# Performance work log

Hardware: AMD Instinct MI355X
Metric: run time of the kernel (lower is better)

The kernel has to match this reference:

```python
import jax, jax.numpy as jnp
import numpy as np

N = 100000
DIM = 128
M = 1600000
E = 200000
HOP = 2


def setup_inputs() -> dict:
    key = jax.random.key(0)
    k1, k2, k3, k4 = jax.random.split(key, 4)
    edge = jax.random.randint(k1, (2, E), 0, N, dtype=jnp.int64)
    adj_row = jax.random.randint(k2, (M,), 0, N, dtype=jnp.int64)
    adj_col = jax.random.randint(k3, (M,), 0, N, dtype=jnp.int64)
    # degree consistent with adjacency rows (clamped to >=1 to avoid 1/0)
    deg = jax.ops.segment_sum(jnp.ones((M,), jnp.float32), adj_row, num_segments=N)
    deg = jnp.maximum(deg, 1.0).reshape(N, 1)
    # 'gaussian' signature sampling: row-L2-normalized standard normal vectors
    g = jax.random.normal(k4, (N, DIM), dtype=jnp.float32)
    x_sig = g / jnp.linalg.norm(g, axis=1, keepdims=True)
    return {"edge": edge, "adj_row": adj_row, "adj_col": adj_col, "deg": deg, "x_sig": x_sig}


def reference(edge, adj_row, adj_col, deg, x_sig):
    n = deg.shape[0]
    D = x_sig.shape[1]
    degrev = 1.0 / deg  # [N,1]
    # x: [N, 3*D] -- raw / rsqrt(deg)-scaled / rsqrt(1+log(deg))-scaled signatures
    x = jnp.concatenate(
        [x_sig, x_sig * jax.lax.rsqrt(deg), x_sig * jax.lax.rsqrt(1.0 + jnp.log(deg))],
        axis=1,
    )

    def spmm(v):  # adj_t @ v via gather + segment-sum over nnz
        return jax.ops.segment_sum(v[adj_col], adj_row, num_segments=n)

    xs = [x, degrev * spmm(x)]
    for _ in range(2, HOP + 1):
        xs.append(degrev * spmm(xs[-1]) - xs[-2])
    # [N, K, D] with K = 3*(hop+1)
    X = jnp.concatenate(xs, axis=1).reshape(n, -1, D)
    a = X[edge[0]]  # [E, K, D]
    b = X[edge[1]]  # [E, K, D]
    ret = jnp.einsum("ekd,eld->ekl", a, b)  # [E, K, K]
    ret = ret + jnp.swapaxes(ret, 1, 2)
    return ret.reshape(ret.shape[0], -1)  # [E, K*K]
```

## Files before the change

kernel.cpp:

```cpp
#include <hip/hip_runtime.h>
#include <hip/hip_fp16.h>

#define D128 128
#define X19_STRIDE 768

typedef __attribute__((ext_vector_type(8))) _Float16 f16x8;
typedef __attribute__((ext_vector_type(4))) float    f32x4;

__global__ void k_scales(const float* __restrict__ deg, float* __restrict__ scales, int N) {
  int n = blockIdx.x * blockDim.x + threadIdx.x;
  if (n >= N) return;
  float dg = deg[n];
  scales[2 * n]     = rsqrtf(dg);
  scales[2 * n + 1] = rsqrtf(1.0f + logf(dg));
}

__global__ void k_hist(const int* __restrict__ row, int* __restrict__ cnt, int M) {
  int i = blockIdx.x * blockDim.x + threadIdx.x;
  if (i < M) atomicAdd(&cnt[row[i]], 1);
}

__global__ void __launch_bounds__(256)
k_blocksum(const int* __restrict__ cnt, int* __restrict__ bsum, int n) {
  __shared__ int ws[4];
  int base = blockIdx.x * 1024;
  int t = threadIdx.x;
  int s = 0;
  for (int j = t; j < 1024; j += 256) {
    int i = base + j;
    if (i < n) s += cnt[i];
  }
  #pragma unroll
  for (int d = 32; d >= 1; d >>= 1) s += __shfl_down(s, d);
  if ((t & 63) == 0) ws[t >> 6] = s;
  __syncthreads();
  if (t == 0) bsum[blockIdx.x] = ws[0] + ws[1] + ws[2] + ws[3];
}

__global__ void k_scan_bsums(const int* __restrict__ bsum, int* __restrict__ bpre,
                             int* __restrict__ off, int nb, int n) {
  if (threadIdx.x == 0 && blockIdx.x == 0) {
    int run = 0;
    for (int b = 0; b < nb; ++b) { bpre[b] = run; run += bsum[b]; }
    off[n] = run;
  }
}

__global__ void __launch_bounds__(1024)
k_scan_apply(const int* __restrict__ cnt, const int* __restrict__ bpre,
             int* __restrict__ off, int* __restrict__ cursor, int n) {
  __shared__ int warp_sums[16];
  int i = blockIdx.x * 1024 + threadIdx.x;
  int lane = threadIdx.x & 63;
  int wid  = threadIdx.x >> 6;
  int v = (i < n) ? cnt[i] : 0;
  int s = v;
  #pragma unroll
  for (int d = 1; d < 64; d <<= 1) {
    int t = __shfl_up(s, d);
    if (lane >= d) s += t;
  }
  if (lane == 63) warp_sums[wid] = s;
  __syncthreads();
  if (threadIdx.x < 16) {
    int ws = warp_sums[threadIdx.x];
    #pragma unroll
    for (int d = 1; d < 16; d <<= 1) {
      int t = __shfl_up(ws, d);
      if ((int)threadIdx.x >= d) ws += t;
    }
    warp_sums[threadIdx.x] = ws;
  }
  __syncthreads();
  int excl = (s - v) + (wid > 0 ? warp_sums[wid - 1] : 0) + bpre[blockIdx.x];
  if (i < n) { off[i] = excl; cursor[i] = excl; }
}

__global__ void k_scatter(const int* __restrict__ row, const int* __restrict__ col,
                          int* __restrict__ cursor, int* __restrict__ csr_col, int M) {
  int i = blockIdx.x * blockDim.x + threadIdx.x;
  if (i < M) {
    int r = row[i];
    int pos = atomicAdd(&cursor[r], 1);
    csr_col[pos] = col[i];
  }
}

__global__ void __launch_bounds__(256)
k_spmm1(const float* __restrict__ x_sig, const float* __restrict__ scales,
        __half* __restrict__ X19,
        const int* __restrict__ off, const int* __restrict__ csr_col,
        const float* __restrict__ deg, int N) {
  int r = blockIdx.x * 4 + (threadIdx.x >> 6);
  if (r >= N) return;
  int lane = threadIdx.x & 63;
  int d0 = lane * 2;
  int start = off[r], end = off[r + 1];
  float a0x = 0.f, a0y = 0.f, a1x = 0.f, a1y = 0.f, a2x = 0.f, a2y = 0.f;
  for (int b = start; b < end; b += 64) {
    int len = min(end - b, 64);
    int ci = (lane < len) ? csr_col[b + lane] : 0;
    for (int j = 0; j < len; ++j) {
      int c = __shfl(ci, j);
      float2 v = *reinterpret_cast<const float2*>(x_sig + (size_t)c * D128 + d0);
      float2 s = *reinterpret_cast<const float2*>(scales + 2 * c);
      a0x += v.x;        a0y += v.y;
      a1x += v.x * s.x;  a1y += v.y * s.x;
      a2x += v.x * s.y;  a2y += v.y * s.y;
    }
  }
  float dr = 1.0f / deg[r];
  __half* o = X19 + (size_t)r * X19_STRIDE + d0;
  *reinterpret_cast<__half2*>(o)       = __floats2half2_rn(a0x * dr, a0y * dr);
  *reinterpret_cast<__half2*>(o + 128) = __floats2half2_rn(a1x * dr, a1y * dr);
  *reinterpret_cast<__half2*>(o + 256) = __floats2half2_rn(a2x * dr, a2y * dr);
}

__global__ void __launch_bounds__(256)
k_spmm2(const float* __restrict__ x_sig, const float* __restrict__ scales,
        __half* __restrict__ X19,
        const int* __restrict__ off, const int* __restrict__ csr_col,
        const float* __restrict__ deg, int N) {
  int r = blockIdx.x * 4 + (threadIdx.x >> 6);
  if (r >= N) return;
  int lane = threadIdx.x & 63;
  int d0 = lane * 2;
  int start = off[r], end = off[r + 1];
  float s0x = 0.f, s0y = 0.f, s1x = 0.f, s1y = 0.f, s2x = 0.f, s2y = 0.f;
  for (int b = start; b < end; b += 64) {
    int len = min(end - b, 64);
    int ci = (lane < len) ? csr_col[b + lane] : 0;
    for (int j = 0; j < len; ++j) {
      int c = __shfl(ci, j);
      const __half* base = X19 + (size_t)c * X19_STRIDE + d0;
      float2 v0 = __half22float2(*reinterpret_cast<const __half2*>(base));
      float2 v1 = __half22float2(*reinterpret_cast<const __half2*>(base + 128));
      float2 v2 = __half22float2(*reinterpret_cast<const __half2*>(base + 256));
      s0x += v0.x; s0y += v0.y;
      s1x += v1.x; s1y += v1.y;
      s2x += v2.x; s2y += v2.y;
    }
  }
  float dr = 1.0f / deg[r];
  float2 xv = *reinterpret_cast<const float2*>(x_sig + (size_t)r * D128 + d0);
  float2 sc = *reinterpret_cast<const float2*>(scales + 2 * r);
  __half* o = X19 + (size_t)r * X19_STRIDE + 384 + d0;
  *reinterpret_cast<__half2*>(o)       = __floats2half2_rn(s0x * dr - xv.x,        s0y * dr - xv.y);
  *reinterpret_cast<__half2*>(o + 128) = __floats2half2_rn(s1x * dr - xv.x * sc.x, s1y * dr - xv.y * sc.x);
  *reinterpret_cast<__half2*>(o + 256) = __floats2half2_rn(s2x * dr - xv.x * sc.y, s2y * dr - xv.y * sc.y);
}

__global__ void __launch_bounds__(256)
k_edge(const float* __restrict__ x_sig, const float* __restrict__ scales,
       const __half* __restrict__ X19, const int* __restrict__ edge,
       float* __restrict__ out, int E) {
  __shared__ float Gs[4][2][49];
  int w    = threadIdx.x >> 6;
  int lane = threadIdx.x & 63;
  long e0 = ((long)blockIdx.x * 4 + w) * 2;
  int row = lane & 15;
  int kg  = lane >> 4;
  int f   = min(row & 7, 6);
  long ea = e0 + ((row >> 3) & 1);
  bool va = ea < E;
  int u = va ? edge[ea] : 0;
  int v = va ? edge[E + ea] : 0;
  const float*  xu = x_sig + (size_t)u * D128;
  const float*  xv = x_sig + (size_t)v * D128;
  const __half* Xu = X19 + (size_t)u * X19_STRIDE + (f - 1) * D128;
  const __half* Xv = X19 + (size_t)v * X19_STRIDE + (f - 1) * D128;

  f32x4 acc = {0.f, 0.f, 0.f, 0.f};
  #pragma unroll
  for (int c = 0; c < 4; ++c) {
    int koff = c * 32 + kg * 8;
    f16x8 a, b;
    if (f == 0) {
      float4 u0 = *reinterpret_cast<const float4*>(xu + koff);
      float4 u1 = *reinterpret_cast<const float4*>(xu + koff + 4);
      float4 v0 = *reinterpret_cast<const float4*>(xv + koff);
      float4 v1 = *reinterpret_cast<const float4*>(xv + koff + 4);
      a[0] = (_Float16)u0.x; a[1] = (_Float16)u0.y; a[2] = (_Float16)u0.z; a[3] = (_Float16)u0.w;
      a[4] = (_Float16)u1.x; a[5] = (_Float16)u1.y; a[6] = (_Float16)u1.z; a[7] = (_Float16)u1.w;
      b[0] = (_Float16)v0.x; b[1] = (_Float16)v0.y; b[2] = (_Float16)v0.z; b[3] = (_Float16)v0.w;
      b[4] = (_Float16)v1.x; b[5] = (_Float16)v1.y; b[6] = (_Float16)v1.z; b[7] = (_Float16)v1.w;
    } else {
      a = *reinterpret_cast<const f16x8*>(Xu + koff);
      b = *reinterpret_cast<const f16x8*>(Xv + koff);
    }
    acc = __builtin_amdgcn_mfma_f32_16x16x32_f16(a, b, acc, 0, 0, 0);
  }
  #pragma unroll
  for (int j = 0; j < 4; ++j) {
    int cr = kg * 4 + j;
    int cc = row;
    if (cr < 7 && cc < 7)                       Gs[w][0][cr * 7 + cc] = acc[j];
    else if (cr >= 8 && cr < 15 && cc >= 8 && cc < 15)
                                                Gs[w][1][(cr - 8) * 7 + (cc - 8)] = acc[j];
  }
  __syncthreads();
  #pragma unroll
  for (int ee = 0; ee < 2; ++ee) {
    long e = e0 + ee;
    if (e >= E) break;
    int uu = edge[e], vv = edge[E + e];
    float su1 = scales[2 * uu], su2 = scales[2 * uu + 1];
    float sv1 = scales[2 * vv], sv2 = scales[2 * vv + 1];
    const float* G = Gs[w][ee];
    for (int t = lane; t < 81; t += 64) {
      int k = t / 9, l = t % 9;
      int kp = (k < 3) ? 0 : k - 2;
      int lp = (l < 3) ? 0 : l - 2;
      float ak = (k == 1) ? su1 : ((k == 2) ? su2 : 1.f);
      float al = (l == 1) ? su1 : ((l == 2) ? su2 : 1.f);
      float bk = (k == 1) ? sv1 : ((k == 2) ? sv2 : 1.f);
      float bl = (l == 1) ? sv1 : ((l == 2) ? sv2 : 1.f);
      out[(size_t)e * 81 + t] = ak * bl * G[kp * 7 + lp] + al * bk * G[lp * 7 + kp];
    }
  }
}

extern "C" void kernel_launch(void* const* d_in, const int* in_sizes, int n_in,
                              void* d_out, int out_size, void* d_ws, size_t ws_size,
                              hipStream_t stream) {
  const int*   edge    = (const int*)d_in[0];
  const int*   adj_row = (const int*)d_in[1];
  const int*   adj_col = (const int*)d_in[2];
  const float* deg     = (const float*)d_in[3];
  const float* x_sig   = (const float*)d_in[4];
  float* out = (float*)d_out;

  const int E = in_sizes[0] / 2;
  const int M = in_sizes[1];
  const int N = in_sizes[3];
  const int NCHUNK = (N + 1023) / 1024;

  size_t x19_elems = (size_t)N * X19_STRIDE;
  size_t need = x19_elems * 2
              + (2 * (size_t)N) * 4
              + ((size_t)(N + 1) + (size_t)N + (size_t)M) * 4
              + 2 * (size_t)NCHUNK * 4;
  if (ws_size < need) return;

  __half* X19   = (__half*)d_ws;
  float* scales = (float*)(X19 + x19_elems);
  int* off      = (int*)(scales + 2 * (size_t)N);
  int* cursor   = off + (N + 1);
  int* csr_col  = cursor + N;
  int* bsum     = csr_col + M;
  int* bpre     = bsum + NCHUNK;

  hipMemsetAsync(cursor, 0, (size_t)N * sizeof(int), stream);

  k_scales<<<(N + 255) / 256, 256, 0, stream>>>(deg, scales, N);
  k_hist<<<(M + 255) / 256, 256, 0, stream>>>(adj_row, cursor, M);
  k_blocksum<<<NCHUNK, 256, 0, stream>>>(cursor, bsum, N);
  k_scan_bsums<<<1, 64, 0, stream>>>(bsum, bpre, off, NCHUNK, N);
  k_scan_apply<<<NCHUNK, 1024, 0, stream>>>(cursor, bpre, off, cursor, N);
  k_scatter<<<(M + 255) / 256, 256, 0, stream>>>(adj_row, adj_col, cursor, csr_col, M);

  k_spmm1<<<(N + 3) / 4, 256, 0, stream>>>(x_sig, scales, X19, off, csr_col, deg, N);
  k_spmm2<<<(N + 3) / 4, 256, 0, stream>>>(x_sig, scales, X19, off, csr_col, deg, N);

  k_edge<<<(E + 7) / 8, 256, 0, stream>>>(x_sig, scales, X19, edge, out, E);
}
```

Before: 759.2 us.

## Pre-convert x_sig to fp16 for SpMM gathers and edge MFMA loads

```diff
diff --git a/kernel.cpp b/kernel.cpp
--- a/kernel.cpp
+++ b/kernel.cpp
@@ -13,6 +13,13 @@
   float dg = deg[n];
   scales[2 * n]     = rsqrtf(dg);
   scales[2 * n + 1] = rsqrtf(1.0f + logf(dg));
+}
+
+__global__ void k_xh(const float* __restrict__ x, __half* __restrict__ xh, int total2) {
+  int i = blockIdx.x * blockDim.x + threadIdx.x;
+  if (i >= total2) return;
+  float2 v = *reinterpret_cast<const float2*>(x + 2 * i);
+  *reinterpret_cast<__half2*>(xh + 2 * i) = __floats2half2_rn(v.x, v.y);
 }
 
 __global__ void k_hist(const int* __restrict__ row, int* __restrict__ cnt, int M) {
@@ -87,8 +94,8 @@
 }
 
 __global__ void __launch_bounds__(256)
-k_spmm1(const float* __restrict__ x_sig, const float* __restrict__ scales,
-        __half* __restrict__ X19,
+k_spmm1(const float* __restrict__ x_sig, const __half* __restrict__ xh, int use_xh,
+        const float* __restrict__ scales, __half* __restrict__ X19,
         const int* __restrict__ off, const int* __restrict__ csr_col,
         const float* __restrict__ deg, int N) {
   int r = blockIdx.x * 4 + (threadIdx.x >> 6);
@@ -100,13 +107,54 @@
   for (int b = start; b < end; b += 64) {
     int len = min(end - b, 64);
     int ci = (lane < len) ? csr_col[b + lane] : 0;
-    for (int j = 0; j < len; ++j) {
-      int c = __shfl(ci, j);
-      float2 v = *reinterpret_cast<const float2*>(x_sig + (size_t)c * D128 + d0);
-      float2 s = *reinterpret_cast<const float2*>(scales + 2 * c);
-      a0x += v.x;        a0y += v.y;
-      a1x += v.x * s.x;  a1y += v.y * s.x;
-      a2x += v.x * s.y;  a2y += v.y * s.y;
+    if (use_xh) {
+      int j = 0;
+      for (; j + 2 <= len; j += 2) {
+        int c0 = __builtin_amdgcn_readlane(ci, j);
+        int c1 = __builtin_amdgcn_readlane(ci, j + 1);
+        float2 v0 = __half22float2(*reinterpret_cast<const __half2*>(xh + (size_t)c0 * D128 + d0));
+        float2 v1 = __half22float2(*reinterpret_cast<const __half2*>(xh + (size_t)c1 * D128 + d0));
+        float2 s0 = *reinterpret_cast<const float2*>(scales + 2 * c0);
+        float2 s1 = *reinterpret_cast<const float2*>(scales + 2 * c1);
+        a0x += v0.x;        a0y += v0.y;
+        a1x += v0.x * s0.x; a1y += v0.y * s0.x;
+        a2x += v0.x * s0.y; a2y += v0.y * s0.y;
+        a0x += v1.x;        a0y += v1.y;
+        a1x += v1.x * s1.x; a1y += v1.y * s1.x;
+        a2x += v1.x * s1.y; a2y += v1.y * s1.y;
+      }
+      if (j < len) {
+        int c = __builtin_amdgcn_readlane(ci, j);
+        float2 v = __half22float2(*reinterpret_cast<const __half2*>(xh + (size_t)c * D128 + d0));
+        float2 s = *reinterpret_cast<const float2*>(scales + 2 * c);
+        a0x += v.x;        a0y += v.y;
+        a1x += v.x * s.x;  a1y += v.y * s.x;
+        a2x += v.x * s.y;  a2y += v.y * s.y;
+      }
+    } else {
+      int j = 0;
+      for (; j + 2 <= len; j += 2) {
+        int c0 = __builtin_amdgcn_readlane(ci, j);
+        int c1 = __builtin_amdgcn_readlane(ci, j + 1);
+        float2 v0 = *reinterpret_cast<const float2*>(x_sig + (size_t)c0 * D128 + d0);
+        float2 v1 = *reinterpret_cast<const float2*>(x_sig + (size_t)c1 * D128 + d0);
+        float2 s0 = *reinterpret_cast<const float2*>(scales + 2 * c0);
+        float2 s1 = *reinterpret_cast<const float2*>(scales + 2 * c1);
+        a0x += v0.x;        a0y += v0.y;
+        a1x += v0.x * s0.x; a1y += v0.y * s0.x;
+        a2x += v0.x * s0.y; a2y += v0.y * s0.y;
+        a0x += v1.x;        a0y += v1.y;
+        a1x += v1.x * s1.x; a1y += v1.y * s1.x;
+        a2x += v1.x * s1.y; a2y += v1.y * s1.y;
+      }
+      if (j < len) {
+        int c = __builtin_amdgcn_readlane(ci, j);
+        float2 v = *reinterpret_cast<const float2*>(x_sig + (size_t)c * D128 + d0);
+        float2 s = *reinterpret_cast<const float2*>(scales + 2 * c);
+        a0x += v.x;        a0y += v.y;
+        a1x += v.x * s.x;  a1y += v.y * s.x;
+        a2x += v.x * s.y;  a2y += v.y * s.y;
+      }
     }
   }
   float dr = 1.0f / deg[r];
@@ -130,15 +178,31 @@
   for (int b = start; b < end; b += 64) {
     int len = min(end - b, 64);
     int ci = (lane < len) ? csr_col[b + lane] : 0;
-    for (int j = 0; j < len; ++j) {
-      int c = __shfl(ci, j);
-      const __half* base = X19 + (size_t)c * X19_STRIDE + d0;
-      float2 v0 = __half22float2(*reinterpret_cast<const __half2*>(base));
-      float2 v1 = __half22float2(*reinterpret_cast<const __half2*>(base + 128));
-      float2 v2 = __half22float2(*reinterpret_cast<const __half2*>(base + 256));
-      s0x += v0.x; s0y += v0.y;
-      s1x += v1.x; s1y += v1.y;
-      s2x += v2.x; s2y += v2.y;
+    int j = 0;
+    for (; j + 2 <= len; j += 2) {
+      int c0 = __builtin_amdgcn_readlane(ci, j);
+      int c1 = __builtin_amdgcn_readlane(ci, j + 1);
+      const __half* p = X19 + (size_t)c0 * X19_STRIDE + d0;
+      const __half* q = X19 + (size_t)c1 * X19_STRIDE + d0;
+      float2 p0 = __half22float2(*reinterpret_cast<const __half2*>(p));
+      float2 p1 = __half22float2(*reinterpret_cast<const __half2*>(p + 128));
+      float2 p2 = __half22float2(*reinterpret_cast<const __half2*>(p + 256));
+      float2 q0 = __half22float2(*reinterpret_cast<const __half2*>(q));
+      float2 q1 = __half22float2(*reinterpret_cast<const __half2*>(q + 128));
+      float2 q2 = __half22float2(*reinterpret_cast<const __half2*>(q + 256));
+      s0x += p0.x + q0.x; s0y += p0.y + q0.y;
+      s1x += p1.x + q1.x; s1y += p1.y + q1.y;
+      s2x += p2.x + q2.x; s2y += p2.y + q2.y;
+    }
+    if (j < len) {
+      int c = __builtin_amdgcn_readlane(ci, j);
+      const __half* p = X19 + (size_t)c * X19_STRIDE + d0;
+      float2 p0 = __half22float2(*reinterpret_cast<const __half2*>(p));
+      float2 p1 = __half22float2(*reinterpret_cast<const __half2*>(p + 128));
+      float2 p2 = __half22float2(*reinterpret_cast<const __half2*>(p + 256));
+      s0x += p0.x; s0y += p0.y;
+      s1x += p1.x; s1y += p1.y;
+      s2x += p2.x; s2y += p2.y;
     }
   }
   float dr = 1.0f / deg[r];
@@ -151,9 +215,9 @@
 }
 
 __global__ void __launch_bounds__(256)
-k_edge(const float* __restrict__ x_sig, const float* __restrict__ scales,
-       const __half* __restrict__ X19, const int* __restrict__ edge,
-       float* __restrict__ out, int E) {
+k_edge(const float* __restrict__ x_sig, const __half* __restrict__ xh, int use_xh,
+       const float* __restrict__ scales, const __half* __restrict__ X19,
+       const int* __restrict__ edge, float* __restrict__ out, int E) {
   __shared__ float Gs[4][2][49];
   int w    = threadIdx.x >> 6;
   int lane = threadIdx.x & 63;
@@ -165,30 +229,44 @@
   bool va = ea < E;
   int u = va ? edge[ea] : 0;
   int v = va ? edge[E + ea] : 0;
-  const float*  xu = x_sig + (size_t)u * D128;
-  const float*  xv = x_sig + (size_t)v * D128;
-  const __half* Xu = X19 + (size_t)u * X19_STRIDE + (f - 1) * D128;
-  const __half* Xv = X19 + (size_t)v * X19_STRIDE + (f - 1) * D128;
 
   f32x4 acc = {0.f, 0.f, 0.f, 0.f};
-  #pragma unroll
-  for (int c = 0; c < 4; ++c) {
-    int koff = c * 32 + kg * 8;
-    f16x8 a, b;
-    if (f == 0) {
-      float4 u0 = *reinterpret_cast<const float4*>(xu + koff);
-      float4 u1 = *reinterpret_cast<const float4*>(xu + koff + 4);
-      float4 v0 = *reinterpret_cast<const float4*>(xv + koff);
-      float4 v1 = *reinterpret_cast<const float4*>(xv + koff + 4);
-      a[0] = (_Float16)u0.x; a[1] = (_Float16)u0.y; a[2] = (_Float16)u0.z; a[3] = (_Float16)u0.w;
-      a[4] = (_Float16)u1.x; a[5] = (_Float16)u1.y; a[6] = (_Float16)u1.z; a[7] = (_Float16)u1.w;
-      b[0] = (_Float16)v0.x; b[1] = (_Float16)v0.y; b[2] = (_Float16)v0.z; b[3] = (_Float16)v0.w;
-      b[4] = (_Float16)v1.x; b[5] = (_Float16)v1.y; b[6] = (_Float16)v1.z; b[7] = (_Float16)v1.w;
-    } else {
-      a = *reinterpret_cast<const f16x8*>(Xu + koff);
-      b = *reinterpret_cast<const f16x8*>(Xv + koff);
-    }
-    acc = __builtin_amdgcn_mfma_f32_16x16x32_f16(a, b, acc, 0, 0, 0);
+  if (use_xh) {
+    const __half* pa = (f == 0) ? xh + (size_t)u * D128
+                                : X19 + (size_t)u * X19_STRIDE + (size_t)(f - 1) * D128;
+    const __half* pb = (f == 0) ? xh + (size_t)v * D128
+                                : X19 + (size_t)v * X19_STRIDE + (size_t)(f - 1) * D128;
+    #pragma unroll
+    for (int c = 0; c < 4; ++c) {
+      int koff = c * 32 + kg * 8;
+      f16x8 a = *reinterpret_cast<const f16x8*>(pa + koff);
+      f16x8 b = *reinterpret_cast<const f16x8*>(pb + koff);
+      acc = __builtin_amdgcn_mfma_f32_16x16x32_f16(a, b, acc, 0, 0, 0);
+    }
+  } else {
+    const float*  xu = x_sig + (size_t)u * D128;
+    const float*  xv = x_sig + (size_t)v * D128;
+    const __half* Xu = X19 + (size_t)u * X19_STRIDE;
+    const __half* Xv = X19 + (size_t)v * X19_STRIDE;
+    #pragma unroll
+    for (int c = 0; c < 4; ++c) {
+      int koff = c * 32 + kg * 8;
+      f16x8 a, b;
+      if (f == 0) {
+        float4 u0 = *reinterpret_cast<const float4*>(xu + koff);
+        float4 u1 = *reinterpret_cast<const float4*>(xu + koff + 4);
+        float4 v0 = *reinterpret_cast<const float4*>(xv + koff);
+        float4 v1 = *reinterpret_cast<const float4*>(xv + koff + 4);
+        a[0] = (_Float16)u0.x; a[1] = (_Float16)u0.y; a[2] = (_Float16)u0.z; a[3] = (_Float16)u0.w;
+        a[4] = (_Float16)u1.x; a[5] = (_Float16)u1.y; a[6] = (_Float16)u1.z; a[7] = (_Float16)u1.w;
+        b[0] = (_Float16)v0.x; b[1] = (_Float16)v0.y; b[2] = (_Float16)v0.z; b[3] = (_Float16)v0.w;
+        b[4] = (_Float16)v1.x; b[5] = (_Float16)v1.y; b[6] = (_Float16)v1.z; b[7] = (_Float16)v1.w;
+      } else {
+        a = *reinterpret_cast<const f16x8*>(Xu + (f - 1) * D128 + koff);
+        b = *reinterpret_cast<const f16x8*>(Xv + (f - 1) * D128 + koff);
+      }
+      acc = __builtin_amdgcn_mfma_f32_16x16x32_f16(a, b, acc, 0, 0, 0);
+    }
   }
   #pragma unroll
   for (int j = 0; j < 4; ++j) {
@@ -236,11 +314,11 @@
   const int NCHUNK = (N + 1023) / 1024;
 
   size_t x19_elems = (size_t)N * X19_STRIDE;
-  size_t need = x19_elems * 2
+  size_t base_need = x19_elems * 2
               + (2 * (size_t)N) * 4
               + ((size_t)(N + 1) + (size_t)N + (size_t)M) * 4
               + 2 * (size_t)NCHUNK * 4;
-  if (ws_size < need) return;
+  if (ws_size < base_need) return;
 
   __half* X19   = (__half*)d_ws;
   float* scales = (float*)(X19 + x19_elems);
@@ -250,17 +328,24 @@
   int* bsum     = csr_col + M;
   int* bpre     = bsum + NCHUNK;
 
+  size_t xh_off   = (base_need + 255) & ~(size_t)255;
+  size_t xh_bytes = (size_t)N * D128 * 2;
+  int use_xh = (ws_size >= xh_off + xh_bytes) ? 1 : 0;
+  __half* xh = use_xh ? (__half*)((char*)d_ws + xh_off) : (__half*)d_ws;
+
   hipMemsetAsync(cursor, 0, (size_t)N * sizeof(int), stream);
 
   k_scales<<<(N + 255) / 256, 256, 0, stream>>>(deg, scales, N);
+  if (use_xh)
+    k_xh<<<(N * 64 + 255) / 256, 256, 0, stream>>>(x_sig, xh, N * 64);
   k_hist<<<(M + 255) / 256, 256, 0, stream>>>(adj_row, cursor, M);
   k_blocksum<<<NCHUNK, 256, 0, stream>>>(cursor, bsum, N);
   k_scan_bsums<<<1, 64, 0, stream>>>(bsum, bpre, off, NCHUNK, N);
   k_scan_apply<<<NCHUNK, 1024, 0, stream>>>(cursor, bpre, off, cursor, N);
   k_scatter<<<(M + 255) / 256, 256, 0, stream>>>(adj_row, adj_col, cursor, csr_col, M);
 
-  k_spmm1<<<(N + 3) / 4, 256, 0, stream>>>(x_sig, scales, X19, off, csr_col, deg, N);
+  k_spmm1<<<(N + 3) / 4, 256, 0, stream>>>(x_sig, xh, use_xh, scales, X19, off, csr_col, deg, N);
   k_spmm2<<<(N + 3) / 4, 256, 0, stream>>>(x_sig, scales, X19, off, csr_col, deg, N);
 
-  k_edge<<<(E + 7) / 8, 256, 0, stream>>>(x_sig, scales, X19, edge, out, E);
-}
+  k_edge<<<(E + 7) / 8, 256, 0, stream>>>(x_sig, xh, use_xh, scales, X19, edge, out, E);
+}
```

Measured after the change: 696.7 us. -8.2%, faster.
